# Performance work log

Hardware: AMD Instinct MI355X
Metric: run time of the kernel (lower is better)

Reference implementation:

```python
import jax, jax.numpy as jnp
import numpy as np


def _graph_conv_mean(x, src, dst, edge_weight, W_rel, W_root, b, num_nodes):
    # messages: gather source features, optionally scale by edge weight
    msg = x[src]  # [E, D]
    if edge_weight is not None:
        msg = msg * edge_weight[:, None]
    # mean aggregation over incoming edges per destination node
    summed = jax.ops.segment_sum(msg, dst, num_segments=num_nodes)  # [N, D]
    count = jax.ops.segment_sum(jnp.ones((src.shape[0],), x.dtype), dst, num_segments=num_nodes)
    mean = summed / jnp.maximum(count, 1.0)[:, None]
    # out = lin_rel(mean) + lin_root(x) + bias
    return mean @ W_rel + x @ W_root + b


def setup_inputs() -> dict:
    key = jax.random.key(0)
    ks = jax.random.split(key, 8)
    N, E, D, H, C = 100000, 1600000, 128, 32, 5
    x = jax.random.normal(ks[0], (N, D), dtype=jnp.float32)
    edge_index = jax.random.randint(ks[1], (2, E), 0, N, dtype=jnp.int64)
    edge_weight = jax.random.uniform(ks[2], (E,), dtype=jnp.float32)
    W_rel1 = jax.random.normal(ks[3], (D, H), dtype=jnp.float32) / np.sqrt(D)
    W_root1 = jax.random.normal(ks[4], (D, H), dtype=jnp.float32) / np.sqrt(D)
    b1 = jnp.zeros((H,), jnp.float32)
    W_rel2 = jax.random.normal(ks[5], (H, C), dtype=jnp.float32) / np.sqrt(H)
    W_root2 = jax.random.normal(ks[6], (H, C), dtype=jnp.float32) / np.sqrt(H)
    b2 = jnp.zeros((C,), jnp.float32)
    return {"x": x, "edge_index": edge_index, "edge_weight": edge_weight,
            "W_rel1": W_rel1, "W_root1": W_root1, "b1": b1,
            "W_rel2": W_rel2, "W_root2": W_root2, "b2": b2}


def reference(x, edge_index, edge_weight, W_rel1, W_root1, b1, W_rel2, W_root2, b2):
    N = x.shape[0]
    src, dst = edge_index[0], edge_index[1]
    # conv1 with edge_weight
    h = _graph_conv_mean(x, src, dst, edge_weight, W_rel1, W_root1, b1, N)
    h = jax.nn.relu(h)
    # dropout is identity at inference (training=False)
    # conv2 without edge_weight
    out = _graph_conv_mean(h, src, dst, None, W_rel2, W_root2, b2, N)
    return jax.nn.log_softmax(out, axis=1)
```

## Files before the change

kernel.cpp:

```cpp
#include <hip/hip_runtime.h>
#include <math.h>

#define N_NODES 100000
#define E_EDGES 1600000
#define D_IN    128
#define H_MID   32
#define C_OUT   5

#define BSHIFT 8
#define BNODES 256
#define NBKT   391
#define NSH    4
#define SCAP   1216
#define BCAPC  (NSH * SCAP)
#define SRC_BITS 17
#define SRC_MASK 0x1FFFF

#define EB     2048
#define NBA    782
#define NMF    1563

#define KP 136

typedef __attribute__((ext_vector_type(8))) short bf16x8;
typedef __attribute__((ext_vector_type(4))) float f32x4;

__device__ inline unsigned f2bf(float f) {
    unsigned u = __float_as_uint(f);
    return (u + 0x7FFFu + ((u >> 16) & 1u)) >> 16;
}
__device__ inline float bflo(unsigned v) { return __uint_as_float((v & 0xFFFFu) << 16); }
__device__ inline float bfhi(unsigned v) { return __uint_as_float(v & 0xFFFF0000u); }
__device__ inline float bf2f(unsigned short u) { return __uint_as_float(((unsigned)u) << 16); }

__global__ void k_prep(const float* __restrict__ Wrel,
                       const float* __restrict__ Wroot,
                       int* __restrict__ cursor4,
                       unsigned short* __restrict__ wt_g) {
    int tid = threadIdx.x;
    for (int i = tid; i < NBKT * NSH; i += 512) cursor4[i] = 0;
    for (int i = tid; i < 64 * 128; i += 512) {
        int n = i >> 7, k = i & 127;
        float v = (n < H_MID) ? Wrel[k * H_MID + n] : Wroot[k * H_MID + (n - H_MID)];
        wt_g[i] = (unsigned short)f2bf(v);
    }
}

__global__ __launch_bounds__(512) void k_front(
    const int* __restrict__ src,
    const int* __restrict__ dst,
    const float* __restrict__ ew,
    int* __restrict__ cursor4,
    int2* __restrict__ staged,
    const float* __restrict__ x,
    const unsigned short* __restrict__ wt_g,
    const float* __restrict__ b1,
    unsigned short* __restrict__ xrelh,
    float* __restrict__ xroot) {
    __shared__ __align__(16) char smem[26752];
    int tid = threadIdx.x;

    if (blockIdx.x < NBA) {
        int2*  ebuf   = (int2*)smem;
        short* bbuf   = (short*)(smem + 16384);
        int*   cnt0   = (int*)(smem + 20480);
        int*   cnt1   = (int*)(smem + 22044);
        int*   lstart = (int*)(smem + 23608);
        int*   gbase  = (int*)(smem + 25172);
        int*   totp   = (int*)(smem + 26736);
        int eBase = blockIdx.x * EB;
        int shard = blockIdx.x & (NSH - 1);
        int half = tid >> 8;
        int* cntH = half ? cnt1 : cnt0;

        if (tid < NBKT) { cnt0[tid] = 0; cnt1[tid] = 0; }
        __syncthreads();

        int b[4], rank[4], packed[4], wbits[4];
        bool valid[4];
        #pragma unroll
        for (int u = 0; u < 4; ++u) {
            int e = eBase + u * 512 + tid;
            valid[u] = (e < E_EDGES);
            b[u] = 0; rank[u] = 0; packed[u] = 0; wbits[u] = 0;
            if (valid[u]) {
                int d = dst[e];
                int s = src[e];
                wbits[u] = __float_as_int(ew[e]);
                b[u] = d >> BSHIFT;
                packed[u] = ((d & (BNODES - 1)) << SRC_BITS) | s;
                rank[u] = atomicAdd(&cntH[b[u]], 1);
            }
        }
        __syncthreads();

        if (tid < 64) {
            int base = tid * 7;
            int loc[7];
            int s = 0;
            #pragma unroll
            for (int k = 0; k < 7; ++k) {
                int idx = base + k;
                int c = (idx < NBKT) ? (cnt0[idx] + cnt1[idx]) : 0;
                loc[k] = s;
                s += c;
            }
            int run = s;
            #pragma unroll
            for (int off = 1; off < 64; off <<= 1) {
                int t = __shfl_up(run, off, 64);
                if (tid >= off) run += t;
            }
            int excl = run - s;
            #pragma unroll
            for (int k = 0; k < 7; ++k) {
                int idx = base + k;
                if (idx < NBKT) lstart[idx] = excl + loc[k];
            }
            if (tid == 63) *totp = run;
        }
        if (tid < NBKT)
            gbase[tid] = atomicAdd(&cursor4[tid * NSH + shard],
                                   cnt0[tid] + cnt1[tid]);
        __syncthreads();
        int total = *totp;

        #pragma unroll
        for (int u = 0; u < 4; ++u) {
            if (valid[u]) {
                int rg = rank[u] + (half ? cnt0[b[u]] : 0);
                int slot = lstart[b[u]] + rg;
                ebuf[slot] = make_int2(packed[u], wbits[u]);
                bbuf[slot] = (short)b[u];
            }
        }
        __syncthreads();

        for (int t = tid; t < total; t += 512) {
            int2 ev = ebuf[t];
            int bb = bbuf[t];
            int gpos = gbase[bb] + (t - lstart[bb]);
            if (gpos < SCAP)
                staged[((size_t)bb * NSH + shard) * SCAP + gpos] = ev;
        }
    } else {
        unsigned short* xs = (unsigned short*)smem;
        int nodeBase = (blockIdx.x - NBA) * 64;

        #pragma unroll
        for (int it = 0; it < 8; ++it) {
            int idx = it * 512 + tid;
            int row = idx >> 6, kp = idx & 63;
            int node = nodeBase + row;
            float2 v = make_float2(0.f, 0.f);
            if (node < N_NODES)
                v = *(const float2*)(x + (size_t)node * D_IN + kp * 2);
            unsigned pk = f2bf(v.x) | (f2bf(v.y) << 16);
            *(unsigned*)(xs + row * KP + kp * 2) = pk;
        }
        __syncthreads();

        int lane = tid & 63;
        int wv = tid >> 6;
        int m = lane & 15;
        int quad = lane >> 4;
        int rowBase = (wv & 3) * 16;
        int ntBase = (wv >> 2) * 2;

        f32x4 acc[2];
        acc[0] = (f32x4){0.f, 0.f, 0.f, 0.f};
        acc[1] = (f32x4){0.f, 0.f, 0.f, 0.f};

        #pragma unroll
        for (int kk = 0; kk < 4; ++kk) {
            int k0 = kk * 32 + quad * 8;
            bf16x8 a = *(const bf16x8*)(xs + (rowBase + m) * KP + k0);
            #pragma unroll
            for (int t = 0; t < 2; ++t) {
                bf16x8 bb = *(const bf16x8*)(wt_g + ((ntBase + t) * 16 + m) * 128 + k0);
                acc[t] = __builtin_amdgcn_mfma_f32_16x16x32_bf16(a, bb, acc[t], 0, 0, 0);
            }
        }

        #pragma unroll
        for (int t = 0; t < 2; ++t) {
            #pragma unroll
            for (int r = 0; r < 4; ++r) {
                int node = nodeBase + rowBase + quad * 4 + r;
                int colg = (ntBase + t) * 16 + m;
                if (node < N_NODES) {
                    if (colg < H_MID) {
                        xrelh[(size_t)node * H_MID + colg] =
                            (unsigned short)f2bf(acc[t][r]);
                    } else {
                        int c = colg - H_MID;
                        xroot[(size_t)node * H_MID + c] = acc[t][r] + b1[c];
                    }
                }
            }
        }
    }
}

__global__ __launch_bounds__(1024) void k_bucket1(
    const int* __restrict__ cursor4,
    const int2* __restrict__ staged,
    const unsigned short* __restrict__ xrelh,
    const float* __restrict__ xroot,
    const float* __restrict__ Wrel2,
    const float* __restrict__ Wroot2,
    const float* __restrict__ b2,
    unsigned short* __restrict__ h2rel8,
    float* __restrict__ h2root,
    int* __restrict__ csr_srcb,
    int* __restrict__ deg_g,
    int* __restrict__ nst_g) {
    __shared__ int2 ecsr[BCAPC];
    __shared__ int hist0[BNODES];
    __shared__ int hist1[BNODES];
    __shared__ int nstart[BNODES];
    __shared__ int cur0[BNODES];
    __shared__ int cur1[BNODES];
    int tid = threadIdx.x;
    int b = blockIdx.x;
    int half = tid >> 9;
    int* histH = half ? hist1 : hist0;
    int* curH  = half ? cur1  : cur0;

    int cs[NSH];
    #pragma unroll
    for (int s = 0; s < NSH; ++s) {
        int c = cursor4[b * NSH + s];
        cs[s] = (c > SCAP) ? SCAP : c;
    }
    const int2* sp = staged + (size_t)b * NSH * SCAP;

    if (tid < BNODES) { hist0[tid] = 0; hist1[tid] = 0; }
    __syncthreads();
    #pragma unroll
    for (int s = 0; s < NSH; ++s)
        for (int i = tid; i < cs[s]; i += 1024)
            atomicAdd(&histH[((unsigned)sp[s * SCAP + i].x) >> SRC_BITS], 1);
    __syncthreads();

    if (tid < 64) {
        int base = tid * 4;
        int loc[4];
        int s = 0;
        #pragma unroll
        for (int k = 0; k < 4; ++k) {
            loc[k] = s;
            s += hist0[base + k] + hist1[base + k];
        }
        int run = s;
        #pragma unroll
        for (int off = 1; off < 64; off <<= 1) {
            int t = __shfl_up(run, off, 64);
            if (tid >= off) run += t;
        }
        int excl = run - s;
        #pragma unroll
        for (int k = 0; k < 4; ++k)
            nstart[base + k] = excl + loc[k];
    }
    __syncthreads();
    if (tid < BNODES) {
        int h0 = hist0[tid];
        cur0[tid] = nstart[tid];
        cur1[tid] = nstart[tid] + h0;
        int node = b * BNODES + tid;
        if (node < N_NODES) {
            deg_g[node] = h0 + hist1[tid];
            nst_g[node] = nstart[tid];
        }
    }
    __syncthreads();

    #pragma unroll
    for (int s = 0; s < NSH; ++s)
        for (int i = tid; i < cs[s]; i += 1024) {
            int2 ev = sp[s * SCAP + i];
            int local = ((unsigned)ev.x) >> SRC_BITS;
            int pos = atomicAdd(&curH[local], 1);
            ecsr[pos] = make_int2(ev.x & SRC_MASK, ev.y);
        }
    __syncthreads();

    int count = cs[0] + cs[1] + cs[2] + cs[3];

    int* outb = csr_srcb + (size_t)b * BCAPC;
    for (int i = tid; i < count; i += 1024)
        outb[i] = ecsr[i].x;

    int g = tid >> 4;
    int lane = tid & 15;
    for (int nl = g; nl < BNODES; nl += 64) {
        int node = b * BNODES + nl;
        if (node >= N_NODES) continue;
        int dg = hist0[nl] + hist1[nl];
        int i = nstart[nl];
        int end = i + dg;

        float acc0 = 0.f, acc1 = 0.f;
        for (; i + 8 <= end; i += 8) {
            int2 e[8];
            unsigned v[8];
            #pragma unroll
            for (int u = 0; u < 8; ++u) e[u] = ecsr[i + u];
            #pragma unroll
            for (int u = 0; u < 8; ++u)
                v[u] = *(const unsigned*)(xrelh + (size_t)e[u].x * H_MID + lane * 2);
            #pragma unroll
            for (int u = 0; u < 8; ++u) {
                float w = __int_as_float(e[u].y);
                acc0 += bflo(v[u]) * w;
                acc1 += bfhi(v[u]) * w;
            }
        }
        for (; i < end; ++i) {
            int2 e0 = ecsr[i];
            unsigned v0 = *(const unsigned*)(xrelh + (size_t)e0.x * H_MID + lane * 2);
            float w0 = __int_as_float(e0.y);
            acc0 += bflo(v0) * w0;
            acc1 += bfhi(v0) * w0;
        }

        float inv = 1.0f / fmaxf((float)dg, 1.0f);
        float2 rt = *(const float2*)(xroot + (size_t)node * H_MID + lane * 2);
        float h0 = fmaxf(acc0 * inv + rt.x, 0.f);
        float h1 = fmaxf(acc1 * inv + rt.y, 0.f);

        float p[2 * C_OUT];
        #pragma unroll
        for (int j = 0; j < C_OUT; ++j) {
            p[j]         = h0 * Wrel2[(2 * lane) * C_OUT + j]
                         + h1 * Wrel2[(2 * lane + 1) * C_OUT + j];
            p[C_OUT + j] = h0 * Wroot2[(2 * lane) * C_OUT + j]
                         + h1 * Wroot2[(2 * lane + 1) * C_OUT + j];
        }
        #pragma unroll
        for (int mm = 8; mm > 0; mm >>= 1) {
            #pragma unroll
            for (int j = 0; j < 2 * C_OUT; ++j)
                p[j] += __shfl_xor(p[j], mm, 16);
        }
        if (lane == 0) {
            #pragma unroll
            for (int j = 0; j < C_OUT; ++j) {
                h2rel8[(size_t)node * 8 + j] = (unsigned short)f2bf(p[j]);
                h2root[(size_t)node * C_OUT + j] = p[C_OUT + j] + b2[j];
            }
        }
    }
}

__global__ __launch_bounds__(256) void k_bucket2(
    const int* __restrict__ deg_g,
    const int* __restrict__ nst_g,
    const int* __restrict__ csr_srcb,
    const unsigned short* __restrict__ h2rel8,
    const float* __restrict__ h2root,
    float* __restrict__ out) {
    int node = blockIdx.x * 32 + (threadIdx.x >> 3);
    int lane = threadIdx.x & 7;
    int dg  = deg_g[node];
    int beg = (node >> BSHIFT) * BCAPC + nst_g[node];
    int end = beg + dg;

    float acc = 0.f;
    if (lane < C_OUT) {
        int i = beg;
        int nfull = dg >> 3;
        if (nfull) {
            int s[8];
            #pragma unroll
            for (int u = 0; u < 8; ++u) s[u] = csr_srcb[i + u];
            for (int bb = 1; bb < nfull; ++bb) {
                float v[8];
                #pragma unroll
                for (int u = 0; u < 8; ++u)
                    v[u] = bf2f(h2rel8[(size_t)s[u] * 8 + lane]);
                int s2[8];
                #pragma unroll
                for (int u = 0; u < 8; ++u) s2[u] = csr_srcb[i + 8 + u];
                #pragma unroll
                for (int u = 0; u < 8; ++u) acc += v[u];
                #pragma unroll
                for (int u = 0; u < 8; ++u) s[u] = s2[u];
                i += 8;
            }
            #pragma unroll
            for (int u = 0; u < 8; ++u)
                acc += bf2f(h2rel8[(size_t)s[u] * 8 + lane]);
            i += 8;
        }
        for (; i < end; ++i)
            acc += bf2f(h2rel8[(size_t)csr_srcb[i] * 8 + lane]);
    }
    float inv = 1.0f / fmaxf((float)dg, 1.0f);
    float o = (lane < C_OUT)
                  ? acc * inv + h2root[(size_t)node * C_OUT + lane]
                  : -INFINITY;
    float m = o;
    #pragma unroll
    for (int dd = 4; dd > 0; dd >>= 1) m = fmaxf(m, __shfl_xor(m, dd, 8));
    float e = (lane < C_OUT) ? expf(o - m) : 0.f;
    float ssum = e;
    #pragma unroll
    for (int dd = 4; dd > 0; dd >>= 1) ssum += __shfl_xor(ssum, dd, 8);
    float lse = m + logf(ssum);
    if (lane < C_OUT)
        out[(size_t)node * C_OUT + lane] = o - lse;
}

extern "C" void kernel_launch(void* const* d_in, const int* in_sizes, int n_in,
                              void* d_out, int out_size, void* d_ws, size_t ws_size,
                              hipStream_t stream) {
    const float* x      = (const float*)d_in[0];
    const int*   ei     = (const int*)d_in[1];
    const float* ew     = (const float*)d_in[2];
    const float* Wrel1  = (const float*)d_in[3];
    const float* Wroot1 = (const float*)d_in[4];
    const float* b1     = (const float*)d_in[5];
    const float* Wrel2  = (const float*)d_in[6];
    const float* Wroot2 = (const float*)d_in[7];
    const float* b2     = (const float*)d_in[8];
    float* out = (float*)d_out;

    const int* src = ei;
    const int* dst = ei + E_EDGES;

    char* ws = (char*)d_ws;
    int*   cursor4       = (int*)ws;
    unsigned short* wt_g = (unsigned short*)(cursor4 + 2048);
    int2*  staged        = (int2*)(wt_g + 64 * 128);
    unsigned short* xrelh = (unsigned short*)(staged + (size_t)NBKT * NSH * SCAP);
    float* xroot         = (float*)(xrelh + (size_t)N_NODES * H_MID);
    unsigned short* h2rel8 = (unsigned short*)(xroot + (size_t)N_NODES * H_MID);
    float* h2root        = (float*)(h2rel8 + (size_t)N_NODES * 8);
    int*   csr_srcb      = (int*)(h2root + (size_t)N_NODES * C_OUT);
    int*   deg_g         = csr_srcb + (size_t)NBKT * BCAPC;
    int*   nst_g         = deg_g + N_NODES;

    k_prep<<<1, 512, 0, stream>>>(Wrel1, Wroot1, cursor4, wt_g);

    k_front<<<NBA + NMF, 512, 0, stream>>>(src, dst, ew, cursor4, staged,
                                           x, wt_g, b1, xrelh, xroot);

    k_bucket1<<<NBKT, 1024, 0, stream>>>(cursor4, staged,
                                         xrelh, xroot, Wrel2, Wroot2, b2,
                                         h2rel8, h2root, csr_srcb, deg_g, nst_g);

    k_bucket2<<<N_NODES / 32, 256, 0, stream>>>(deg_g, nst_g, csr_srcb,
                                                h2rel8, h2root, out);
}
```

Baseline: 205.9 us.

## Replace global atomic bucket scatter with per-block sorted segments and descriptors

The front kernel no longer reserves space in global per-bucket shards with atomics. Each edge block now writes its locally bucket-sorted edges contiguously, plus a descriptor table of bucket start offsets. The bucket kernel then has each of its first 782 threads walk its own source block's segment for that bucket. This removes the global atomics, the scattered writes and the cursor reset, but each thread reads a short serial run of about four edges from a different segment, so the reads are uncoalesced and latency-bound.

Measured after the change: 212.8 us. +3.3%, slower.

```diff
diff --git a/kernel.cpp b/kernel.cpp
--- a/kernel.cpp
+++ b/kernel.cpp
@@ -10,15 +10,14 @@
 #define BSHIFT 8
 #define BNODES 256
 #define NBKT   391
-#define NSH    4
-#define SCAP   1216
-#define BCAPC  (NSH * SCAP)
+#define ECAP   4864
 #define SRC_BITS 17
 #define SRC_MASK 0x1FFFF
 
 #define EB     2048
 #define NBA    782
 #define NMF    1563
+#define NDESC  392
 
 #define KP 136
 
@@ -35,10 +34,8 @@
 
 __global__ void k_prep(const float* __restrict__ Wrel,
                        const float* __restrict__ Wroot,
-                       int* __restrict__ cursor4,
                        unsigned short* __restrict__ wt_g) {
     int tid = threadIdx.x;
-    for (int i = tid; i < NBKT * NSH; i += 512) cursor4[i] = 0;
     for (int i = tid; i < 64 * 128; i += 512) {
         int n = i >> 7, k = i & 127;
         float v = (n < H_MID) ? Wrel[k * H_MID + n] : Wroot[k * H_MID + (n - H_MID)];
@@ -50,26 +47,23 @@
     const int* __restrict__ src,
     const int* __restrict__ dst,
     const float* __restrict__ ew,
-    int* __restrict__ cursor4,
-    int2* __restrict__ staged,
+    int2* __restrict__ staged2,
+    int* __restrict__ desc,
     const float* __restrict__ x,
     const unsigned short* __restrict__ wt_g,
     const float* __restrict__ b1,
     unsigned short* __restrict__ xrelh,
     float* __restrict__ xroot) {
-    __shared__ __align__(16) char smem[26752];
+    __shared__ __align__(16) char smem[21504];
     int tid = threadIdx.x;
 
     if (blockIdx.x < NBA) {
         int2*  ebuf   = (int2*)smem;
-        short* bbuf   = (short*)(smem + 16384);
-        int*   cnt0   = (int*)(smem + 20480);
-        int*   cnt1   = (int*)(smem + 22044);
-        int*   lstart = (int*)(smem + 23608);
-        int*   gbase  = (int*)(smem + 25172);
-        int*   totp   = (int*)(smem + 26736);
+        int*   cnt0   = (int*)(smem + 16384);
+        int*   cnt1   = (int*)(smem + 17948);
+        int*   lstart = (int*)(smem + 19512);
+        int*   totp   = (int*)(smem + 21076);
         int eBase = blockIdx.x * EB;
-        int shard = blockIdx.x & (NSH - 1);
         int half = tid >> 8;
         int* cntH = half ? cnt1 : cnt0;
 
@@ -119,9 +113,6 @@
             }
             if (tid == 63) *totp = run;
         }
-        if (tid < NBKT)
-            gbase[tid] = atomicAdd(&cursor4[tid * NSH + shard],
-                                   cnt0[tid] + cnt1[tid]);
         __syncthreads();
         int total = *totp;
 
@@ -131,18 +122,15 @@
                 int rg = rank[u] + (half ? cnt0[b[u]] : 0);
                 int slot = lstart[b[u]] + rg;
                 ebuf[slot] = make_int2(packed[u], wbits[u]);
-                bbuf[slot] = (short)b[u];
             }
         }
         __syncthreads();
 
-        for (int t = tid; t < total; t += 512) {
-            int2 ev = ebuf[t];
-            int bb = bbuf[t];
-            int gpos = gbase[bb] + (t - lstart[bb]);
-            if (gpos < SCAP)
-                staged[((size_t)bb * NSH + shard) * SCAP + gpos] = ev;
-        }
+        int2* outp = staged2 + (size_t)blockIdx.x * EB;
+        for (int t = tid; t < total; t += 512)
+            outp[t] = ebuf[t];
+        if (tid < NDESC)
+            desc[blockIdx.x * NDESC + tid] = (tid < NBKT) ? lstart[tid] : total;
     } else {
         unsigned short* xs = (unsigned short*)smem;
         int nodeBase = (blockIdx.x - NBA) * 64;
@@ -203,8 +191,8 @@
 }
 
 __global__ __launch_bounds__(1024) void k_bucket1(
-    const int* __restrict__ cursor4,
-    const int2* __restrict__ staged,
+    const int2* __restrict__ staged2,
+    const int* __restrict__ desc,
     const unsigned short* __restrict__ xrelh,
     const float* __restrict__ xroot,
     const float* __restrict__ Wrel2,
@@ -215,7 +203,7 @@
     int* __restrict__ csr_srcb,
     int* __restrict__ deg_g,
     int* __restrict__ nst_g) {
-    __shared__ int2 ecsr[BCAPC];
+    __shared__ int2 ecsr[ECAP];
     __shared__ int hist0[BNODES];
     __shared__ int hist1[BNODES];
     __shared__ int nstart[BNODES];
@@ -227,38 +215,36 @@
     int* histH = half ? hist1 : hist0;
     int* curH  = half ? cur1  : cur0;
 
-    int cs[NSH];
-    #pragma unroll
-    for (int s = 0; s < NSH; ++s) {
-        int c = cursor4[b * NSH + s];
-        cs[s] = (c > SCAP) ? SCAP : c;
-    }
-    const int2* sp = staged + (size_t)b * NSH * SCAP;
-
     if (tid < BNODES) { hist0[tid] = 0; hist1[tid] = 0; }
+
+    int s = 0, e = 0;
+    const int2* myseg = staged2 + (size_t)tid * EB;
+    if (tid < NBA) {
+        s = desc[tid * NDESC + b];
+        e = desc[tid * NDESC + b + 1];
+    }
     __syncthreads();
-    #pragma unroll
-    for (int s = 0; s < NSH; ++s)
-        for (int i = tid; i < cs[s]; i += 1024)
-            atomicAdd(&histH[((unsigned)sp[s * SCAP + i].x) >> SRC_BITS], 1);
+
+    for (int i = s; i < e; ++i)
+        atomicAdd(&histH[((unsigned)myseg[i].x) >> SRC_BITS], 1);
     __syncthreads();
 
     if (tid < 64) {
         int base = tid * 4;
         int loc[4];
-        int s = 0;
+        int sv = 0;
         #pragma unroll
         for (int k = 0; k < 4; ++k) {
-            loc[k] = s;
-            s += hist0[base + k] + hist1[base + k];
-        }
-        int run = s;
+            loc[k] = sv;
+            sv += hist0[base + k] + hist1[base + k];
+        }
+        int run = sv;
         #pragma unroll
         for (int off = 1; off < 64; off <<= 1) {
             int t = __shfl_up(run, off, 64);
             if (tid >= off) run += t;
         }
-        int excl = run - s;
+        int excl = run - sv;
         #pragma unroll
         for (int k = 0; k < 4; ++k)
             nstart[base + k] = excl + loc[k];
@@ -276,19 +262,19 @@
     }
     __syncthreads();
 
-    #pragma unroll
-    for (int s = 0; s < NSH; ++s)
-        for (int i = tid; i < cs[s]; i += 1024) {
-            int2 ev = sp[s * SCAP + i];
-            int local = ((unsigned)ev.x) >> SRC_BITS;
-            int pos = atomicAdd(&curH[local], 1);
+    for (int i = s; i < e; ++i) {
+        int2 ev = myseg[i];
+        int local = ((unsigned)ev.x) >> SRC_BITS;
+        int pos = atomicAdd(&curH[local], 1);
+        if (pos < ECAP)
             ecsr[pos] = make_int2(ev.x & SRC_MASK, ev.y);
-        }
+    }
     __syncthreads();
 
-    int count = cs[0] + cs[1] + cs[2] + cs[3];
-
-    int* outb = csr_srcb + (size_t)b * BCAPC;
+    int count = nstart[BNODES - 1] + hist0[BNODES - 1] + hist1[BNODES - 1];
+    if (count > ECAP) count = ECAP;
+
+    int* outb = csr_srcb + (size_t)b * ECAP;
     for (int i = tid; i < count; i += 1024)
         outb[i] = ecsr[i].x;
 
@@ -303,16 +289,16 @@
 
         float acc0 = 0.f, acc1 = 0.f;
         for (; i + 8 <= end; i += 8) {
-            int2 e[8];
+            int2 ee[8];
             unsigned v[8];
             #pragma unroll
-            for (int u = 0; u < 8; ++u) e[u] = ecsr[i + u];
+            for (int u = 0; u < 8; ++u) ee[u] = ecsr[i + u];
             #pragma unroll
             for (int u = 0; u < 8; ++u)
-                v[u] = *(const unsigned*)(xrelh + (size_t)e[u].x * H_MID + lane * 2);
+                v[u] = *(const unsigned*)(xrelh + (size_t)ee[u].x * H_MID + lane * 2);
             #pragma unroll
             for (int u = 0; u < 8; ++u) {
-                float w = __int_as_float(e[u].y);
+                float w = __int_as_float(ee[u].y);
                 acc0 += bflo(v[u]) * w;
                 acc1 += bfhi(v[u]) * w;
             }
@@ -364,7 +350,7 @@
     int node = blockIdx.x * 32 + (threadIdx.x >> 3);
     int lane = threadIdx.x & 7;
     int dg  = deg_g[node];
-    int beg = (node >> BSHIFT) * BCAPC + nst_g[node];
+    int beg = (node >> BSHIFT) * ECAP + nst_g[node];
     int end = beg + dg;
 
     float acc = 0.f;
@@ -431,23 +417,23 @@
     const int* dst = ei + E_EDGES;
 
     char* ws = (char*)d_ws;
-    int*   cursor4       = (int*)ws;
-    unsigned short* wt_g = (unsigned short*)(cursor4 + 2048);
-    int2*  staged        = (int2*)(wt_g + 64 * 128);
-    unsigned short* xrelh = (unsigned short*)(staged + (size_t)NBKT * NSH * SCAP);
+    unsigned short* wt_g = (unsigned short*)ws;
+    int2*  staged2       = (int2*)(wt_g + 64 * 128);
+    int*   desc          = (int*)(staged2 + (size_t)NBA * EB);
+    unsigned short* xrelh = (unsigned short*)(desc + (size_t)NBA * NDESC);
     float* xroot         = (float*)(xrelh + (size_t)N_NODES * H_MID);
     unsigned short* h2rel8 = (unsigned short*)(xroot + (size_t)N_NODES * H_MID);
     float* h2root        = (float*)(h2rel8 + (size_t)N_NODES * 8);
     int*   csr_srcb      = (int*)(h2root + (size_t)N_NODES * C_OUT);
-    int*   deg_g         = csr_srcb + (size_t)NBKT * BCAPC;
+    int*   deg_g         = csr_srcb + (size_t)NBKT * ECAP;
     int*   nst_g         = deg_g + N_NODES;
 
-    k_prep<<<1, 512, 0, stream>>>(Wrel1, Wroot1, cursor4, wt_g);
-
-    k_front<<<NBA + NMF, 512, 0, stream>>>(src, dst, ew, cursor4, staged,
+    k_prep<<<1, 512, 0, stream>>>(Wrel1, Wroot1, wt_g);
+
+    k_front<<<NBA + NMF, 512, 0, stream>>>(src, dst, ew, staged2, desc,
                                            x, wt_g, b1, xrelh, xroot);
 
-    k_bucket1<<<NBKT, 1024, 0, stream>>>(cursor4, staged,
+    k_bucket1<<<NBKT, 1024, 0, stream>>>(staged2, desc,
                                          xrelh, xroot, Wrel2, Wroot2, b2,
                                          h2rel8, h2root, csr_srcb, deg_g, nst_g);
 
```
